# Optimization experiments

Measured on AMD Instinct MI355X. Metric: run time of the kernel, lower is better.

The kernel has to match this reference:

```python
import jax, jax.numpy as jnp
import numpy as np

N = 100000   # nodes
E = 600000   # edges
IN = 12      # in_dim
H = 128      # hidden_dim
OUT = 2      # out_dim
L = 3        # num_layers
EPS = 1e-5   # BatchNorm eps


def setup_inputs() -> dict:
    key = jax.random.key(0)
    ks = jax.random.split(key, 14)
    s = 0.05
    return {
        "features": jax.random.normal(ks[0], (N, IN), jnp.float32),
        "edge_index": jax.random.randint(ks[1], (2, E), 0, N, dtype=jnp.int32).astype(jnp.int64),
        "emb_W": jax.random.normal(ks[2], (IN, H), jnp.float32) * s,
        "emb_b": jnp.zeros((H,), jnp.float32),
        "Wself": jax.random.normal(ks[3], (L, H, H), jnp.float32) * s,
        "Wneigh": jax.random.normal(ks[4], (L, H, H), jnp.float32) * s,
        "conv_b": jnp.zeros((L, H), jnp.float32),
        "bn_gamma": jnp.ones((L, H), jnp.float32),
        "bn_beta": jnp.zeros((L, H), jnp.float32),
        "W1": jax.random.normal(ks[5], (H, H // 2), jnp.float32) * s,
        "b1": jnp.zeros((H // 2,), jnp.float32),
        "W2": jax.random.normal(ks[6], (H // 2, OUT), jnp.float32) * s,
        "b2": jnp.zeros((OUT,), jnp.float32),
    }


def reference(features, edge_index, emb_W, emb_b, Wself, Wneigh, conv_b,
              bn_gamma, bn_beta, W1, b1, W2, b2):
    src, dst = edge_index[0], edge_index[1]
    # in-degree per destination node (loop-invariant)
    deg = jax.ops.segment_sum(jnp.ones((E,), features.dtype), dst, num_segments=N)
    inv_deg = 1.0 / jnp.maximum(deg, 1.0)  # [N]

    h = features @ emb_W + emb_b           # embedding: [N, H]
    h_last = h
    for i in range(L):
        # SAGEConv 'mean': gather src feats, scatter-sum to dst, divide by degree
        msg_sum = jax.ops.segment_sum(h[src], dst, num_segments=N)  # [N, H]
        h_neigh = msg_sum * inv_deg[:, None]
        h_new = h @ Wself[i] + h_neigh @ Wneigh[i] + conv_b[i]
        # BatchNorm1d over nodes (batch statistics)
        mu = jnp.mean(h_new, axis=0)
        var = jnp.var(h_new, axis=0)
        h_new = (h_new - mu) * jax.lax.rsqrt(var + EPS) * bn_gamma[i] + bn_beta[i]
        h_new = jax.nn.relu(h_new)
        # dropout is identity at inference
        if i > 0:
            h_new = h_new + h_last  # residual
        h_last = h_new
        h = h_new
    # MLP head
    out = jax.nn.relu(h @ W1 + b1) @ W2 + b2  # [N, 2]
    return out
```

## Files before the change

### kernel.cpp

```cpp
#include <hip/hip_runtime.h>
#include <hip/hip_bf16.h>
#include <cstdint>

#define H 128
#define EPS 1e-5f
#define CAP 32
#define NB 16

typedef unsigned int uint;
typedef unsigned short ushort;
typedef short short8 __attribute__((ext_vector_type(8)));
typedef float f32x4 __attribute__((ext_vector_type(4)));

__device__ __forceinline__ ushort f2bf(float f) {
  uint u = __float_as_uint(f);
  u += 0x7fffu + ((u >> 16) & 1u);
  return (ushort)(u >> 16);
}
__device__ __forceinline__ float bflo(uint v) { return __uint_as_float(v << 16); }
__device__ __forceinline__ float bfhi(uint v) { return __uint_as_float(v & 0xffff0000u); }

__device__ __forceinline__ int load_idx(const void* ei, long long pos, int is64) {
  if (is64) return (int)((const long long*)ei)[pos];
  return ((const int*)ei)[pos];
}

__global__ __launch_bounds__(256) void k_init(const void* __restrict__ ei, int N,
                                              uint* __restrict__ cnt, int* __restrict__ flag,
                                              const float* __restrict__ F, const float* __restrict__ embW,
                                              const float* __restrict__ embB,
                                              ushort* __restrict__ bufA, ushort* __restrict__ bufB,
                                              const float* __restrict__ Wself, const float* __restrict__ Wneigh,
                                              const float* __restrict__ W1,
                                              ushort* __restrict__ Wsw, ushort* __restrict__ W1sw,
                                              int ZB, int EB) {
  __shared__ float sW[12 * 128];
  __shared__ float sF[256 * 12];
  int b = blockIdx.x, t = threadIdx.x;
  if (b < ZB) {
    int i = b * 256 + t;
    if (i < N) cnt[i] = 0u;
    if (b == 0 && t == 0) {
      const long long* p = (const long long*)ei;
      int ok = 1;
      for (int j = 0; j < 16; ++j) {
        long long s = p[j];
        if (s < 0 || s >= (long long)N) ok = 0;
      }
      *flag = ok;
    }
    return;
  }
  if (b < ZB + EB) {
    int blk = b - ZB;
    for (int i = t; i < 12 * 128; i += 256) sW[i] = embW[i];
    int row0 = blk * 256;
    int nrows = min(256, N - row0);
    for (int i = t; i < nrows * 12; i += 256) sF[i] = F[(size_t)row0 * 12 + i];
    __syncthreads();
    int col = t & 127, half = t >> 7;
    float bias = embB[col];
    int rlo = half * 128, rhi = min(nrows, rlo + 128);
    for (int r = rlo; r < rhi; ++r) {
      float acc = bias;
#pragma unroll
      for (int k = 0; k < 12; ++k) acc = fmaf(sF[r * 12 + k], sW[k * 128 + col], acc);
      bufA[(size_t)(row0 + r) * H + col] = f2bf(acc);
    }
    if (blk == 0 && t < 128) {
      bufA[(size_t)N * H + t] = 0;
      bufB[(size_t)N * H + t] = 0;
    }
    return;
  }
  int e = (b - ZB - EB) * 256 + t;
  if (e < 3 * 4096) {
    int l = e >> 12, r = e & 4095;
    int kt = r >> 9, nt = (r >> 6) & 7, lane = r & 63;
    int quad = lane >> 4, l16 = lane & 15;
    int n = nt * 16 + l16;
    ushort* dst = Wsw + ((size_t)l * 4096 + (kt * 8 + nt) * 64 + lane) * 8;
#pragma unroll
    for (int j = 0; j < 8; ++j) {
      int k = kt * 32 + quad * 8 + j;
      float v = (k < 128) ? Wself[(size_t)l * H * H + (size_t)k * H + n]
                          : Wneigh[(size_t)l * H * H + (size_t)(k - 128) * H + n];
      dst[j] = f2bf(v);
    }
  } else if (e < 3 * 4096 + 1024) {
    int r = e - 3 * 4096;
    int kt = r >> 8, nt = (r >> 6) & 3, lane = r & 63;
    int quad = lane >> 4, l16 = lane & 15;
    int n = nt * 16 + l16;
    ushort* dst = W1sw + ((size_t)((kt * 4 + nt) * 64 + lane)) * 8;
#pragma unroll
    for (int j = 0; j < 8; ++j) {
      int k = kt * 32 + quad * 8 + j;
      dst[j] = f2bf(W1[(size_t)k * 64 + n]);
    }
  }
}

__global__ __launch_bounds__(256) void k_fill(const void* __restrict__ ei, uint* __restrict__ cnt,
                                              uint* __restrict__ csr, int E,
                                              const int* __restrict__ flag) {
  int e0 = (blockIdx.x * 256 + threadIdx.x) * 2;
  if (e0 >= E) return;
  int is64 = *flag;
  int s0, s1 = -1, d0, d1 = -1;
  bool two = (e0 + 1 < E);
  if (is64) {
    const unsigned long long* p = (const unsigned long long*)ei;
    if (two) {
      ulong2 sv = *(const ulong2*)(p + e0);
      ulong2 dv = *(const ulong2*)(p + E + e0);
      s0 = (int)sv.x; s1 = (int)sv.y; d0 = (int)dv.x; d1 = (int)dv.y;
    } else {
      s0 = (int)p[e0]; d0 = (int)p[E + e0];
    }
  } else {
    const int* p = (const int*)ei;
    if (two) {
      int2 sv = *(const int2*)(p + e0);
      int2 dv = *(const int2*)(p + E + e0);
      s0 = sv.x; s1 = sv.y; d0 = dv.x; d1 = dv.y;
    } else {
      s0 = p[e0]; d0 = p[E + e0];
    }
  }
  uint p0 = atomicAdd(&cnt[d0], 1u);
  if (p0 < (uint)CAP) csr[(size_t)d0 * CAP + p0] = (uint)s0;
  if (two) {
    uint p1 = atomicAdd(&cnt[d1], 1u);
    if (p1 < (uint)CAP) csr[(size_t)d1 * CAP + p1] = (uint)s1;
  }
}

__global__ __launch_bounds__(256) void k_gather(const ushort* __restrict__ h, ushort* __restrict__ msg,
                                                const uint* __restrict__ cnt,
                                                const uint* __restrict__ csr,
                                                float* __restrict__ bn_acc, int N) {
  int tid = threadIdx.x;
  if (blockIdx.x == 0) {
#pragma unroll
    for (int i = tid; i < NB * 256; i += 256) bn_acc[i] = 0.f;
  }
  int lane = tid & 63, wave = tid >> 6;
  int group = lane >> 4, l16 = lane & 15;
  int n = blockIdx.x * 16 + wave * 4 + group;
  if (n >= N) return;
  uint rawc = cnt[n];
  uint deg = min(rawc, (uint)CAP);
  const uint* row = csr + (size_t)n * CAP;
  const uint4* hu = (const uint4*)h;
  float a0 = 0.f, a1 = 0.f, a2 = 0.f, a3 = 0.f, a4 = 0.f, a5 = 0.f, a6 = 0.f, a7 = 0.f;
  for (uint k = 0; k < deg; k += 8) {
    uint idx[8];
#pragma unroll
    for (int j = 0; j < 8; ++j) idx[j] = (k + j < deg) ? row[k + j] : (uint)N;
    uint4 v[8];
#pragma unroll
    for (int j = 0; j < 8; ++j) v[j] = hu[(size_t)idx[j] * 16 + l16];
#pragma unroll
    for (int j = 0; j < 8; ++j) {
      a0 += bflo(v[j].x); a1 += bfhi(v[j].x);
      a2 += bflo(v[j].y); a3 += bfhi(v[j].y);
      a4 += bflo(v[j].z); a5 += bfhi(v[j].z);
      a6 += bflo(v[j].w); a7 += bfhi(v[j].w);
    }
  }
  float inv = 1.0f / (float)max(rawc, 1u);
  uint4 o;
  o.x = (uint)f2bf(a0 * inv) | ((uint)f2bf(a1 * inv) << 16);
  o.y = (uint)f2bf(a2 * inv) | ((uint)f2bf(a3 * inv) << 16);
  o.z = (uint)f2bf(a4 * inv) | ((uint)f2bf(a5 * inv) << 16);
  o.w = (uint)f2bf(a6 * inv) | ((uint)f2bf(a7 * inv) << 16);
  ((uint4*)msg)[(size_t)n * 16 + l16] = o;
}

__global__ __launch_bounds__(256, 4) void k_gemm(const ushort* __restrict__ hA, ushort* __restrict__ msgz,
                                                 const ushort* __restrict__ Wsw,
                                                 const float* __restrict__ bias,
                                                 float* __restrict__ bn_acc, int N) {
  __shared__ ushort sB[2048 * 8];
  int tid = threadIdx.x;
  int wave = tid >> 6, lane = tid & 63, quad = lane >> 4, l16 = lane & 15;
  const uint4* wsrc = (const uint4*)Wsw;
  uint4* dst = (uint4*)sB;
  uint4 w2[8];
  {
#pragma unroll
    for (int i = 0; i < 8; ++i) dst[i * 256 + tid] = wsrc[i * 256 + tid];
#pragma unroll
    for (int i = 0; i < 8; ++i) w2[i] = wsrc[2048 + i * 256 + tid];
  }
  __syncthreads();

  int wrow0 = blockIdx.x * 128 + wave * 32;
  f32x4 acc[2][8];
#pragma unroll
  for (int m = 0; m < 2; ++m)
#pragma unroll
    for (int nt = 0; nt < 8; ++nt) acc[m][nt] = (f32x4){0.f, 0.f, 0.f, 0.f};

  short8 zf8 = {0, 0, 0, 0, 0, 0, 0, 0};
#pragma unroll
  for (int kt = 0; kt < 4; ++kt) {
    int colb = kt * 32 + quad * 8;
    short8 a[2];
#pragma unroll
    for (int m = 0; m < 2; ++m) {
      int row = wrow0 + m * 16 + l16;
      a[m] = (row < N) ? *(const short8*)(hA + (size_t)row * H + colb) : zf8;
    }
#pragma unroll
    for (int nt = 0; nt < 8; ++nt) {
      short8 bfr = *(const short8*)(sB + ((kt * 8 + nt) * 64 + lane) * 8);
#pragma unroll
      for (int m = 0; m < 2; ++m)
        acc[m][nt] = __builtin_amdgcn_mfma_f32_16x16x32_bf16(a[m], bfr, acc[m][nt], 0, 0, 0);
    }
  }
  __syncthreads();
  {
#pragma unroll
    for (int i = 0; i < 8; ++i) dst[i * 256 + tid] = w2[i];
  }
  __syncthreads();
#pragma unroll
  for (int kt = 0; kt < 4; ++kt) {
    int colb = kt * 32 + quad * 8;
    short8 a[2];
#pragma unroll
    for (int m = 0; m < 2; ++m) {
      int row = wrow0 + m * 16 + l16;
      a[m] = (row < N) ? *(const short8*)(msgz + (size_t)row * H + colb) : zf8;
    }
#pragma unroll
    for (int nt = 0; nt < 8; ++nt) {
      short8 bfr = *(const short8*)(sB + ((kt * 8 + nt) * 64 + lane) * 8);
#pragma unroll
      for (int m = 0; m < 2; ++m)
        acc[m][nt] = __builtin_amdgcn_mfma_f32_16x16x32_bf16(a[m], bfr, acc[m][nt], 0, 0, 0);
    }
  }

  float bs[8];
#pragma unroll
  for (int nt = 0; nt < 8; ++nt) bs[nt] = bias[nt * 16 + l16];
  float ps[8], pq[8];
#pragma unroll
  for (int nt = 0; nt < 8; ++nt) { ps[nt] = 0.f; pq[nt] = 0.f; }
#pragma unroll
  for (int m = 0; m < 2; ++m) {
#pragma unroll
    for (int nt = 0; nt < 8; ++nt) {
      int col = nt * 16 + l16;
#pragma unroll
      for (int r = 0; r < 4; ++r) {
        int row = wrow0 + m * 16 + quad * 4 + r;
        if (row < N) {
          float v = acc[m][nt][r] + bs[nt];
          msgz[(size_t)row * H + col] = f2bf(v);
          ps[nt] += v; pq[nt] += v * v;
        }
      }
    }
  }
  __syncthreads();
  float* red = (float*)sB;
  int wq = wave * 4 + quad;
#pragma unroll
  for (int nt = 0; nt < 8; ++nt) {
    red[(wq * 8 + nt) * 17 + l16] = ps[nt];
    red[2176 + (wq * 8 + nt) * 17 + l16] = pq[nt];
  }
  __syncthreads();
  if (tid < 128) {
    int nt = tid >> 4, lc = tid & 15;
    float s = 0.f, q = 0.f;
#pragma unroll
    for (int w2i = 0; w2i < 16; ++w2i) {
      s += red[(w2i * 8 + nt) * 17 + lc];
      q += red[2176 + (w2i * 8 + nt) * 17 + lc];
    }
    float* bank = bn_acc + (size_t)(blockIdx.x & (NB - 1)) * 256;
    atomicAdd(&bank[tid], s);
    atomicAdd(&bank[128 + tid], q);
  }
}

__global__ __launch_bounds__(256) void k_norm(uint4* __restrict__ z, const uint4* __restrict__ hprev,
                                              const float* __restrict__ bn_acc,
                                              const float* __restrict__ gamma,
                                              const float* __restrict__ beta,
                                              int residual, int n4, float invN) {
  __shared__ float ssc[128], ssh[128];
  int t = threadIdx.x;
  if (t < 128) {
    float s = 0.f, q = 0.f;
#pragma unroll
    for (int b = 0; b < NB; ++b) {
      s += bn_acc[b * 256 + t];
      q += bn_acc[b * 256 + 128 + t];
    }
    float mu = s * invN;
    float var = fmaxf(q * invN - mu * mu, 0.f);
    float sc = gamma[t] * rsqrtf(var + EPS);
    ssc[t] = sc;
    ssh[t] = beta[t] - mu * sc;
  }
  __syncthreads();
  int idx = blockIdx.x * 256 + t;
  if (idx >= n4) return;
  int j = (idx & 15) * 8;
  uint4 v = z[idx];
  float x0 = fmaxf(fmaf(bflo(v.x), ssc[j + 0], ssh[j + 0]), 0.f);
  float x1 = fmaxf(fmaf(bfhi(v.x), ssc[j + 1], ssh[j + 1]), 0.f);
  float x2 = fmaxf(fmaf(bflo(v.y), ssc[j + 2], ssh[j + 2]), 0.f);
  float x3 = fmaxf(fmaf(bfhi(v.y), ssc[j + 3], ssh[j + 3]), 0.f);
  float x4 = fmaxf(fmaf(bflo(v.z), ssc[j + 4], ssh[j + 4]), 0.f);
  float x5 = fmaxf(fmaf(bfhi(v.z), ssc[j + 5], ssh[j + 5]), 0.f);
  float x6 = fmaxf(fmaf(bflo(v.w), ssc[j + 6], ssh[j + 6]), 0.f);
  float x7 = fmaxf(fmaf(bfhi(v.w), ssc[j + 7], ssh[j + 7]), 0.f);
  if (residual) {
    uint4 r = hprev[idx];
    x0 += bflo(r.x); x1 += bfhi(r.x); x2 += bflo(r.y); x3 += bfhi(r.y);
    x4 += bflo(r.z); x5 += bfhi(r.z); x6 += bflo(r.w); x7 += bfhi(r.w);
  }
  uint4 o;
  o.x = (uint)f2bf(x0) | ((uint)f2bf(x1) << 16);
  o.y = (uint)f2bf(x2) | ((uint)f2bf(x3) << 16);
  o.z = (uint)f2bf(x4) | ((uint)f2bf(x5) << 16);
  o.w = (uint)f2bf(x6) | ((uint)f2bf(x7) << 16);
  z[idx] = o;
}

__global__ __launch_bounds__(256) void k_head(const ushort* __restrict__ z, const ushort* __restrict__ hprev,
                                              const float* __restrict__ bn_acc,
                                              const float* __restrict__ gamma,
                                              const float* __restrict__ beta, float invN,
                                              const ushort* __restrict__ W1sw,
                                              const float* __restrict__ b1, const float* __restrict__ W2,
                                              const float* __restrict__ b2, float* __restrict__ out, int N) {
  __shared__ float ssc[128], ssh[128];
  int tid = threadIdx.x;
  if (tid < 128) {
    float s = 0.f, q = 0.f;
#pragma unroll
    for (int b = 0; b < NB; ++b) {
      s += bn_acc[b * 256 + tid];
      q += bn_acc[b * 256 + 128 + tid];
    }
    float mu = s * invN;
    float var = fmaxf(q * invN - mu * mu, 0.f);
    float sc = gamma[tid] * rsqrtf(var + EPS);
    ssc[tid] = sc;
    ssh[tid] = beta[tid] - mu * sc;
  }
  __syncthreads();
  int wave = tid >> 6, lane = tid & 63, quad = lane >> 4, l16 = lane & 15;
  int wrow0 = blockIdx.x * 64 + wave * 16;
  int am = wrow0 + l16;
  bool avalid = am < N;
  short8 af[4];
#pragma unroll
  for (int kt = 0; kt < 4; ++kt) {
    int c0 = kt * 32 + quad * 8;
    uint4 vz = avalid ? ((const uint4*)z)[(size_t)am * 16 + kt * 4 + quad] : make_uint4(0, 0, 0, 0);
    uint4 vr = avalid ? ((const uint4*)hprev)[(size_t)am * 16 + kt * 4 + quad] : make_uint4(0, 0, 0, 0);
    float x0 = fmaxf(fmaf(bflo(vz.x), ssc[c0 + 0], ssh[c0 + 0]), 0.f) + bflo(vr.x);
    float x1 = fmaxf(fmaf(bfhi(vz.x), ssc[c0 + 1], ssh[c0 + 1]), 0.f) + bfhi(vr.x);
    float x2 = fmaxf(fmaf(bflo(vz.y), ssc[c0 + 2], ssh[c0 + 2]), 0.f) + bflo(vr.y);
    float x3 = fmaxf(fmaf(bfhi(vz.y), ssc[c0 + 3], ssh[c0 + 3]), 0.f) + bfhi(vr.y);
    float x4 = fmaxf(fmaf(bflo(vz.z), ssc[c0 + 4], ssh[c0 + 4]), 0.f) + bflo(vr.z);
    float x5 = fmaxf(fmaf(bfhi(vz.z), ssc[c0 + 5], ssh[c0 + 5]), 0.f) + bfhi(vr.z);
    float x6 = fmaxf(fmaf(bflo(vz.w), ssc[c0 + 6], ssh[c0 + 6]), 0.f) + bflo(vr.w);
    float x7 = fmaxf(fmaf(bfhi(vz.w), ssc[c0 + 7], ssh[c0 + 7]), 0.f) + bfhi(vr.w);
    ushort u[8] = {f2bf(x0), f2bf(x1), f2bf(x2), f2bf(x3), f2bf(x4), f2bf(x5), f2bf(x6), f2bf(x7)};
    af[kt] = *(short8*)u;
  }
  const short8* Bp = (const short8*)W1sw;
  f32x4 acc[4];
#pragma unroll
  for (int nt = 0; nt < 4; ++nt) acc[nt] = (f32x4){0.f, 0.f, 0.f, 0.f};
#pragma unroll
  for (int kt = 0; kt < 4; ++kt) {
#pragma unroll
    for (int nt = 0; nt < 4; ++nt) {
      short8 bfr = Bp[(kt * 4 + nt) * 64 + lane];
      acc[nt] = __builtin_amdgcn_mfma_f32_16x16x32_bf16(af[kt], bfr, acc[nt], 0, 0, 0);
    }
  }
  float p0[4] = {0.f, 0.f, 0.f, 0.f}, p1[4] = {0.f, 0.f, 0.f, 0.f};
#pragma unroll
  for (int nt = 0; nt < 4; ++nt) {
    int c = nt * 16 + l16;
    float bc = b1[c], w20 = W2[c * 2], w21 = W2[c * 2 + 1];
#pragma unroll
    for (int r = 0; r < 4; ++r) {
      float v = fmaxf(acc[nt][r] + bc, 0.f);
      p0[r] = fmaf(v, w20, p0[r]);
      p1[r] = fmaf(v, w21, p1[r]);
    }
  }
#pragma unroll
  for (int m = 1; m < 16; m <<= 1) {
#pragma unroll
    for (int r = 0; r < 4; ++r) {
      p0[r] += __shfl_xor(p0[r], m);
      p1[r] += __shfl_xor(p1[r], m);
    }
  }
  if (l16 == 0) {
    float b20 = b2[0], b21 = b2[1];
#pragma unroll
    for (int r = 0; r < 4; ++r) {
      int row = wrow0 + quad * 4 + r;
      if (row < N) {
        float2 o = make_float2(p0[r] + b20, p1[r] + b21);
        *(float2*)(out + (size_t)row * 2) = o;
      }
    }
  }
}

extern "C" void kernel_launch(void* const* d_in, const int* in_sizes, int n_in,
                              void* d_out, int out_size, void* d_ws, size_t ws_size,
                              hipStream_t stream) {
  const float* features = (const float*)d_in[0];
  const void*  edges    = d_in[1];
  const float* emb_W    = (const float*)d_in[2];
  const float* emb_b    = (const float*)d_in[3];
  const float* Wself    = (const float*)d_in[4];
  const float* Wneigh   = (const float*)d_in[5];
  const float* conv_b   = (const float*)d_in[6];
  const float* bn_gamma = (const float*)d_in[7];
  const float* bn_beta  = (const float*)d_in[8];
  const float* W1       = (const float*)d_in[9];
  const float* b1       = (const float*)d_in[10];
  const float* W2       = (const float*)d_in[11];
  const float* b2       = (const float*)d_in[12];
  float* out = (float*)d_out;
  const int N = in_sizes[0] / 12;
  const int E = in_sizes[1] / 2;
  const float invN = 1.0f / (float)N;

  char* ws = (char*)d_ws;
  size_t off = 0;
  auto take = [&](size_t bytes) {
    char* p = ws + off;
    off = (off + bytes + 511) & ~(size_t)511;
    return p;
  };
  int*    flag   = (int*)take(4);
  uint*   cnt    = (uint*)take((size_t)N * 4);
  uint*   csr    = (uint*)take((size_t)N * CAP * 4);
  float*  bn_acc = (float*)take(NB * 256 * 4);
  ushort* Wsw    = (ushort*)take(3 * 4096 * 8 * 2);
  ushort* W1sw   = (ushort*)take(1024 * 8 * 2);
  ushort* bufA   = (ushort*)take(((size_t)N + 1) * H * 2);
  ushort* bufB   = (ushort*)take(((size_t)N + 1) * H * 2);

  const int ZB = (N + 255) / 256;
  const int EB = (N + 255) / 256;
  const int PB = (3 * 4096 + 1024 + 255) / 256;
  const int FB = (E + 511) / 512;
  const int GB = (N + 127) / 128;

  k_init<<<ZB + EB + PB, 256, 0, stream>>>(edges, N, cnt, flag, features, emb_W, emb_b,
                                           bufA, bufB, Wself, Wneigh, W1, Wsw, W1sw, ZB, EB);
  k_fill<<<FB, 256, 0, stream>>>(edges, cnt, csr, E, flag);

  ushort* hbuf = bufA;
  ushort* obuf = bufB;
  const int n4 = N * 16;
  for (int i = 0; i < 3; ++i) {
    k_gather<<<(N + 15) / 16, 256, 0, stream>>>(hbuf, obuf, cnt, csr, bn_acc, N);
    k_gemm<<<GB, 256, 0, stream>>>(hbuf, obuf, Wsw + (size_t)i * 4096 * 8,
                                   conv_b + (size_t)i * H, bn_acc, N);
    if (i < 2) {
      k_norm<<<(n4 + 255) / 256, 256, 0, stream>>>((uint4*)obuf, (const uint4*)hbuf, bn_acc,
                                                   bn_gamma + (size_t)i * H, bn_beta + (size_t)i * H,
                                                   (i > 0) ? 1 : 0, n4, invN);
      ushort* t = hbuf; hbuf = obuf; obuf = t;
    }
  }
  k_head<<<(N + 63) / 64, 256, 0, stream>>>(obuf, hbuf, bn_acc, bn_gamma + 2 * H, bn_beta + 2 * H,
                                            invN, W1sw, b1, W2, b2, out, N);
}
```

Before: 357.5 us.

## Fuse neighbor gather into the SAGE GEMM kernel via swizzled LDS tile

Merges the mean-aggregation gather kernel and the dual GEMM kernel into one kernel. Each block gathers its 128 nodes' neighbor means straight into a swizzled shared-memory tile, so the message matrix is never written to or reread from global memory. Weights are now read from global/L2 rather than staged in LDS. The BN accumulator zeroing moves into the init kernel, with a separate bank per layer. The cost is a heavier kernel whose latency-bound gather phase may limit occupancy and overlap with the MFMA phase.

```diff
diff --git a/kernel.cpp b/kernel.cpp
--- a/kernel.cpp
+++ b/kernel.cpp
@@ -19,11 +19,6 @@
 }
 __device__ __forceinline__ float bflo(uint v) { return __uint_as_float(v << 16); }
 __device__ __forceinline__ float bfhi(uint v) { return __uint_as_float(v & 0xffff0000u); }
-
-__device__ __forceinline__ int load_idx(const void* ei, long long pos, int is64) {
-  if (is64) return (int)((const long long*)ei)[pos];
-  return ((const int*)ei)[pos];
-}
 
 __global__ __launch_bounds__(256) void k_init(const void* __restrict__ ei, int N,
                                               uint* __restrict__ cnt, int* __restrict__ flag,
@@ -33,6 +28,7 @@
                                               const float* __restrict__ Wself, const float* __restrict__ Wneigh,
                                               const float* __restrict__ W1,
                                               ushort* __restrict__ Wsw, ushort* __restrict__ W1sw,
+                                              float* __restrict__ bn_all,
                                               int ZB, int EB) {
   __shared__ float sW[12 * 128];
   __shared__ float sF[256 * 12];
@@ -40,14 +36,17 @@
   if (b < ZB) {
     int i = b * 256 + t;
     if (i < N) cnt[i] = 0u;
-    if (b == 0 && t == 0) {
-      const long long* p = (const long long*)ei;
-      int ok = 1;
-      for (int j = 0; j < 16; ++j) {
-        long long s = p[j];
-        if (s < 0 || s >= (long long)N) ok = 0;
+    if (b == 0) {
+      for (int j = t; j < NB * 256 * 3; j += 256) bn_all[j] = 0.f;
+      if (t == 0) {
+        const long long* p = (const long long*)ei;
+        int ok = 1;
+        for (int j = 0; j < 16; ++j) {
+          long long s = p[j];
+          if (s < 0 || s >= (long long)N) ok = 0;
+        }
+        *flag = ok;
       }
-      *flag = ok;
     }
     return;
   }
@@ -136,74 +135,63 @@
   }
 }
 
-__global__ __launch_bounds__(256) void k_gather(const ushort* __restrict__ h, ushort* __restrict__ msg,
-                                                const uint* __restrict__ cnt,
-                                                const uint* __restrict__ csr,
-                                                float* __restrict__ bn_acc, int N) {
-  int tid = threadIdx.x;
-  if (blockIdx.x == 0) {
-#pragma unroll
-    for (int i = tid; i < NB * 256; i += 256) bn_acc[i] = 0.f;
-  }
-  int lane = tid & 63, wave = tid >> 6;
-  int group = lane >> 4, l16 = lane & 15;
-  int n = blockIdx.x * 16 + wave * 4 + group;
-  if (n >= N) return;
-  uint rawc = cnt[n];
-  uint deg = min(rawc, (uint)CAP);
-  const uint* row = csr + (size_t)n * CAP;
-  const uint4* hu = (const uint4*)h;
-  float a0 = 0.f, a1 = 0.f, a2 = 0.f, a3 = 0.f, a4 = 0.f, a5 = 0.f, a6 = 0.f, a7 = 0.f;
-  for (uint k = 0; k < deg; k += 8) {
-    uint idx[8];
-#pragma unroll
-    for (int j = 0; j < 8; ++j) idx[j] = (k + j < deg) ? row[k + j] : (uint)N;
-    uint4 v[8];
-#pragma unroll
-    for (int j = 0; j < 8; ++j) v[j] = hu[(size_t)idx[j] * 16 + l16];
-#pragma unroll
-    for (int j = 0; j < 8; ++j) {
-      a0 += bflo(v[j].x); a1 += bfhi(v[j].x);
-      a2 += bflo(v[j].y); a3 += bfhi(v[j].y);
-      a4 += bflo(v[j].z); a5 += bfhi(v[j].z);
-      a6 += bflo(v[j].w); a7 += bfhi(v[j].w);
-    }
-  }
-  float inv = 1.0f / (float)max(rawc, 1u);
-  uint4 o;
-  o.x = (uint)f2bf(a0 * inv) | ((uint)f2bf(a1 * inv) << 16);
-  o.y = (uint)f2bf(a2 * inv) | ((uint)f2bf(a3 * inv) << 16);
-  o.z = (uint)f2bf(a4 * inv) | ((uint)f2bf(a5 * inv) << 16);
-  o.w = (uint)f2bf(a6 * inv) | ((uint)f2bf(a7 * inv) << 16);
-  ((uint4*)msg)[(size_t)n * 16 + l16] = o;
-}
-
-__global__ __launch_bounds__(256, 4) void k_gemm(const ushort* __restrict__ hA, ushort* __restrict__ msgz,
-                                                 const ushort* __restrict__ Wsw,
-                                                 const float* __restrict__ bias,
-                                                 float* __restrict__ bn_acc, int N) {
-  __shared__ ushort sB[2048 * 8];
+__global__ __launch_bounds__(256, 4) void k_gg(const ushort* __restrict__ h, ushort* __restrict__ z,
+                                               const uint* __restrict__ cnt, const uint* __restrict__ csr,
+                                               const ushort* __restrict__ Wsw, const float* __restrict__ bias,
+                                               float* __restrict__ bn_acc, int N) {
+  __shared__ ushort sMsg[128 * 128];
   int tid = threadIdx.x;
   int wave = tid >> 6, lane = tid & 63, quad = lane >> 4, l16 = lane & 15;
-  const uint4* wsrc = (const uint4*)Wsw;
-  uint4* dst = (uint4*)sB;
-  uint4 w2[8];
+  int row0 = blockIdx.x * 128;
+
   {
-#pragma unroll
-    for (int i = 0; i < 8; ++i) dst[i * 256 + tid] = wsrc[i * 256 + tid];
-#pragma unroll
-    for (int i = 0; i < 8; ++i) w2[i] = wsrc[2048 + i * 256 + tid];
-  }
-  __syncthreads();
-
-  int wrow0 = blockIdx.x * 128 + wave * 32;
+    const uint4* hu = (const uint4*)h;
+#pragma unroll
+    for (int p = 0; p < 8; ++p) {
+      int nl = p * 16 + wave * 4 + quad;
+      int n = row0 + nl;
+      uint rawc = (n < N) ? cnt[n] : 0u;
+      uint deg = min(rawc, (uint)CAP);
+      const uint* row = csr + (size_t)n * CAP;
+      float a0 = 0.f, a1 = 0.f, a2 = 0.f, a3 = 0.f, a4 = 0.f, a5 = 0.f, a6 = 0.f, a7 = 0.f;
+      for (uint k = 0; k < deg; k += 8) {
+        uint4 r0 = *(const uint4*)(row + k);
+        uint4 r1 = *(const uint4*)(row + k + 4);
+        uint raw[8] = {r0.x, r0.y, r0.z, r0.w, r1.x, r1.y, r1.z, r1.w};
+        uint idx[8];
+#pragma unroll
+        for (int j = 0; j < 8; ++j) idx[j] = (k + j < deg) ? raw[j] : (uint)N;
+        uint4 v[8];
+#pragma unroll
+        for (int j = 0; j < 8; ++j) v[j] = hu[(size_t)idx[j] * 16 + l16];
+#pragma unroll
+        for (int j = 0; j < 8; ++j) {
+          a0 += bflo(v[j].x); a1 += bfhi(v[j].x);
+          a2 += bflo(v[j].y); a3 += bfhi(v[j].y);
+          a4 += bflo(v[j].z); a5 += bfhi(v[j].z);
+          a6 += bflo(v[j].w); a7 += bfhi(v[j].w);
+        }
+      }
+      float inv = 1.0f / (float)max(rawc, 1u);
+      uint4 o;
+      o.x = (uint)f2bf(a0 * inv) | ((uint)f2bf(a1 * inv) << 16);
+      o.y = (uint)f2bf(a2 * inv) | ((uint)f2bf(a3 * inv) << 16);
+      o.z = (uint)f2bf(a4 * inv) | ((uint)f2bf(a5 * inv) << 16);
+      o.w = (uint)f2bf(a6 * inv) | ((uint)f2bf(a7 * inv) << 16);
+      int off = nl * 256 + ((l16 * 16) ^ ((nl & 7) << 4));
+      *(uint4*)((char*)sMsg + off) = o;
+    }
+  }
+
+  int wrow0 = row0 + wave * 32;
   f32x4 acc[2][8];
 #pragma unroll
   for (int m = 0; m < 2; ++m)
 #pragma unroll
     for (int nt = 0; nt < 8; ++nt) acc[m][nt] = (f32x4){0.f, 0.f, 0.f, 0.f};
-
   short8 zf8 = {0, 0, 0, 0, 0, 0, 0, 0};
+  const short8* Bp = (const short8*)Wsw;
+
 #pragma unroll
   for (int kt = 0; kt < 4; ++kt) {
     int colb = kt * 32 + quad * 8;
@@ -211,34 +199,29 @@
 #pragma unroll
     for (int m = 0; m < 2; ++m) {
       int row = wrow0 + m * 16 + l16;
-      a[m] = (row < N) ? *(const short8*)(hA + (size_t)row * H + colb) : zf8;
+      a[m] = (row < N) ? *(const short8*)(h + (size_t)row * H + colb) : zf8;
     }
 #pragma unroll
     for (int nt = 0; nt < 8; ++nt) {
-      short8 bfr = *(const short8*)(sB + ((kt * 8 + nt) * 64 + lane) * 8);
+      short8 bfr = Bp[(kt * 8 + nt) * 64 + lane];
 #pragma unroll
       for (int m = 0; m < 2; ++m)
         acc[m][nt] = __builtin_amdgcn_mfma_f32_16x16x32_bf16(a[m], bfr, acc[m][nt], 0, 0, 0);
     }
   }
   __syncthreads();
-  {
-#pragma unroll
-    for (int i = 0; i < 8; ++i) dst[i * 256 + tid] = w2[i];
-  }
-  __syncthreads();
-#pragma unroll
-  for (int kt = 0; kt < 4; ++kt) {
-    int colb = kt * 32 + quad * 8;
+#pragma unroll
+  for (int kt = 4; kt < 8; ++kt) {
+    int cb = (kt - 4) * 64 + quad * 16;
     short8 a[2];
 #pragma unroll
     for (int m = 0; m < 2; ++m) {
-      int row = wrow0 + m * 16 + l16;
-      a[m] = (row < N) ? *(const short8*)(msgz + (size_t)row * H + colb) : zf8;
+      int rl = wave * 32 + m * 16 + l16;
+      a[m] = *(const short8*)((const char*)sMsg + rl * 256 + (cb ^ ((l16 & 7) << 4)));
     }
 #pragma unroll
     for (int nt = 0; nt < 8; ++nt) {
-      short8 bfr = *(const short8*)(sB + ((kt * 8 + nt) * 64 + lane) * 8);
+      short8 bfr = Bp[(kt * 8 + nt) * 64 + lane];
 #pragma unroll
       for (int m = 0; m < 2; ++m)
         acc[m][nt] = __builtin_amdgcn_mfma_f32_16x16x32_bf16(a[m], bfr, acc[m][nt], 0, 0, 0);
@@ -261,14 +244,14 @@
         int row = wrow0 + m * 16 + quad * 4 + r;
         if (row < N) {
           float v = acc[m][nt][r] + bs[nt];
-          msgz[(size_t)row * H + col] = f2bf(v);
+          z[(size_t)row * H + col] = f2bf(v);
           ps[nt] += v; pq[nt] += v * v;
         }
       }
     }
   }
   __syncthreads();
-  float* red = (float*)sB;
+  float* red = (float*)sMsg;
   int wq = wave * 4 + quad;
 #pragma unroll
   for (int nt = 0; nt < 8; ++nt) {
@@ -456,7 +439,7 @@
   int*    flag   = (int*)take(4);
   uint*   cnt    = (uint*)take((size_t)N * 4);
   uint*   csr    = (uint*)take((size_t)N * CAP * 4);
-  float*  bn_acc = (float*)take(NB * 256 * 4);
+  float*  bn_all = (float*)take(NB * 256 * 3 * 4);
   ushort* Wsw    = (ushort*)take(3 * 4096 * 8 * 2);
   ushort* W1sw   = (ushort*)take(1024 * 8 * 2);
   ushort* bufA   = (ushort*)take(((size_t)N + 1) * H * 2);
@@ -469,23 +452,24 @@
   const int GB = (N + 127) / 128;
 
   k_init<<<ZB + EB + PB, 256, 0, stream>>>(edges, N, cnt, flag, features, emb_W, emb_b,
-                                           bufA, bufB, Wself, Wneigh, W1, Wsw, W1sw, ZB, EB);
+                                           bufA, bufB, Wself, Wneigh, W1, Wsw, W1sw, bn_all, ZB, EB);
   k_fill<<<FB, 256, 0, stream>>>(edges, cnt, csr, E, flag);
 
   ushort* hbuf = bufA;
   ushort* obuf = bufB;
   const int n4 = N * 16;
   for (int i = 0; i < 3; ++i) {
-    k_gather<<<(N + 15) / 16, 256, 0, stream>>>(hbuf, obuf, cnt, csr, bn_acc, N);
-    k_gemm<<<GB, 256, 0, stream>>>(hbuf, obuf, Wsw + (size_t)i * 4096 * 8,
-                                   conv_b + (size_t)i * H, bn_acc, N);
+    float* bn_i = bn_all + (size_t)i * NB * 256;
+    k_gg<<<GB, 256, 0, stream>>>(hbuf, obuf, cnt, csr, Wsw + (size_t)i * 4096 * 8,
+                                 conv_b + (size_t)i * H, bn_i, N);
     if (i < 2) {
-      k_norm<<<(n4 + 255) / 256, 256, 0, stream>>>((uint4*)obuf, (const uint4*)hbuf, bn_acc,
+      k_norm<<<(n4 + 255) / 256, 256, 0, stream>>>((uint4*)obuf, (const uint4*)hbuf, bn_i,
                                                    bn_gamma + (size_t)i * H, bn_beta + (size_t)i * H,
                                                    (i > 0) ? 1 : 0, n4, invN);
       ushort* t = hbuf; hbuf = obuf; obuf = t;
     }
   }
-  k_head<<<(N + 63) / 64, 256, 0, stream>>>(obuf, hbuf, bn_acc, bn_gamma + 2 * H, bn_beta + 2 * H,
+  k_head<<<(N + 63) / 64, 256, 0, stream>>>(obuf, hbuf, bn_all + (size_t)2 * NB * 256,
+                                            bn_gamma + 2 * H, bn_beta + 2 * H,
                                             invN, W1sw, b1, W2, b2, out, N);
 }
```

Measured after the change: 309.7 us. -13.4%, faster.
